# Kernel tuning notes

Hardware: AMD Instinct MI355X
Metric: run time of the kernel (lower is better)

Reference implementation:

```python
import jax, jax.numpy as jnp
import numpy as np

DIM = 192
BASE = 10000.0
DIM_X = DIM // 3
DIM_Y = DIM // 3
DIM_T = DIM - 2 * (DIM // 3)


def _inv_freq(d):
    return 1.0 / (BASE ** (jnp.arange(0, d, 2, dtype=jnp.float32) / d))


def setup_inputs() -> dict:
    key = jax.random.key(0)
    frames, height, width = 32, 64, 64
    x = jax.random.normal(key, (1, frames * height * width, DIM), dtype=jnp.float32)
    return {"x": x, "height": height, "width": width, "frames": frames}


def reference(x, height, width, frames):
    dtype = x.dtype
    # per-axis angle tables: [len, dim_axis/2] -> duplicated to [len, dim_axis]
    fx = jnp.arange(width, dtype=jnp.float32)[:, None] * _inv_freq(DIM_X)[None, :]
    fy = jnp.arange(height, dtype=jnp.float32)[:, None] * _inv_freq(DIM_Y)[None, :]
    ft = jnp.arange(frames, dtype=jnp.float32)[:, None] * _inv_freq(DIM_T)[None, :]
    fx = jnp.concatenate([fx, fx], axis=-1)  # [W, DIM_X]
    fy = jnp.concatenate([fy, fy], axis=-1)  # [H, DIM_Y]
    ft = jnp.concatenate([ft, ft], axis=-1)  # [T, DIM_T]

    def grid(ax, ay, at):
        # broadcast each axis table over the (T, H, W) grid, concat on feature dim
        gx = jnp.broadcast_to(ax[None, None, :, :], (frames, height, width, DIM_X))
        gy = jnp.broadcast_to(ay[None, :, None, :], (frames, height, width, DIM_Y))
        gt = jnp.broadcast_to(at[:, None, None, :], (frames, height, width, DIM_T))
        return jnp.concatenate([gx, gy, gt], axis=-1).reshape(frames * height * width, DIM)

    cos_3d = grid(jnp.cos(fx), jnp.cos(fy), jnp.cos(ft)).astype(dtype)
    sin_3d = grid(jnp.sin(fx), jnp.sin(fy), jnp.sin(ft)).astype(dtype)
    return (cos_3d, sin_3d)
```

## Files before the change

### kernel.cpp

```cpp
#include <hip/hip_runtime.h>


#define NPOS (32 * 64 * 64)
#define DIM 192

#define NEG_C (-0.41524101186092027f)
#define LOG2_INV_2PI (-2.6514961294723187f)
#define R1 0.7498942093324559f
#define R2 0.5623413251903491f
#define R3 0.4216965034285822f

__global__ __launch_bounds__(256) void rope3d_kernel(float* __restrict__ out) {
    const unsigned int i = blockIdx.x * 256u + threadIdx.x;
    const unsigned int r = i / 48u;
    const unsigned int c = i - r * 48u;

    const unsigned int t = r >> 12;
    const unsigned int h = (r >> 6) & 63u;
    const unsigned int w = r & 63u;

    const unsigned int axis = c >> 4;
    const float pos = (float)(axis == 0 ? w : (axis == 1 ? h : t));

    const unsigned int inner0 = (c * 4u) & 31u;
    const float fr0 = __builtin_exp2f(fmaf((float)inner0, NEG_C, LOG2_INV_2PI));
    const float fr1 = fr0 * R1;
    const float fr2 = fr0 * R2;
    const float fr3 = fr0 * R3;

    const float a0 = __builtin_amdgcn_fractf(pos * fr0);
    const float a1 = __builtin_amdgcn_fractf(pos * fr1);
    const float a2 = __builtin_amdgcn_fractf(pos * fr2);
    const float a3 = __builtin_amdgcn_fractf(pos * fr3);

    const float c0 = __builtin_amdgcn_cosf(a0);
    const float c1 = __builtin_amdgcn_cosf(a1);
    const float c2 = __builtin_amdgcn_cosf(a2);
    const float c3 = __builtin_amdgcn_cosf(a3);
    const float s0 = __builtin_amdgcn_sinf(a0);
    const float s1 = __builtin_amdgcn_sinf(a1);
    const float s2 = __builtin_amdgcn_sinf(a2);
    const float s3 = __builtin_amdgcn_sinf(a3);

    const size_t base = (size_t)i * 4u;
    *(float4*)(out + base) = make_float4(c0, c1, c2, c3);
    *(float4*)(out + (size_t)NPOS * DIM + base) = make_float4(s0, s1, s2, s3);
}

extern "C" void kernel_launch(void* const* d_in, const int* in_sizes, int n_in,
                              void* d_out, int out_size, void* d_ws, size_t ws_size,
                              hipStream_t stream) {
    (void)d_in; (void)in_sizes; (void)n_in; (void)d_ws; (void)ws_size; (void)out_size;
    float* out = (float*)d_out;
    const unsigned int total4 = NPOS * 48u;
    const unsigned int blocks = total4 / 256u;
    rope3d_kernel<<<blocks, 256, 0, stream>>>(out);
}
```

Before: 243.1 us.

## Use grid-stride loop reusing x/y sin-cos values across frame strides

Launches a fixed grid of 1536 blocks that loop over the output with a stride of two frames. The x and y axis angles are invariant under that stride, so their sin/cos are computed once and reused; only the time-axis columns recompute, with position advanced by two. This cuts transcendental work and block launch overhead, at the cost of a serial store loop per thread and less parallelism per store.

```diff
diff --git a/kernel.cpp b/kernel.cpp
--- a/kernel.cpp
+++ b/kernel.cpp
@@ -3,6 +3,11 @@
 
 #define NPOS (32 * 64 * 64)
 #define DIM 192
+#define TOTAL4 (NPOS * 48)
+#define NBLK 1536
+#define NTHR 256
+#define GSIZE (NBLK * NTHR)
+#define ITERS (TOTAL4 / GSIZE)
 
 #define NEG_C (-0.41524101186092027f)
 #define LOG2_INV_2PI (-2.6514961294723187f)
@@ -10,17 +15,11 @@
 #define R2 0.5623413251903491f
 #define R3 0.4216965034285822f
 
-__global__ __launch_bounds__(256) void rope3d_kernel(float* __restrict__ out) {
-    const unsigned int i = blockIdx.x * 256u + threadIdx.x;
-    const unsigned int r = i / 48u;
-    const unsigned int c = i - r * 48u;
-
-    const unsigned int t = r >> 12;
-    const unsigned int h = (r >> 6) & 63u;
-    const unsigned int w = r & 63u;
-
+__global__ __launch_bounds__(NTHR) void rope3d_kernel(float* __restrict__ out) {
+    const unsigned int g = blockIdx.x * NTHR + threadIdx.x;
+    const unsigned int r0 = g / 48u;
+    const unsigned int c = g - r0 * 48u;
     const unsigned int axis = c >> 4;
-    const float pos = (float)(axis == 0 ? w : (axis == 1 ? h : t));
 
     const unsigned int inner0 = (c * 4u) & 31u;
     const float fr0 = __builtin_exp2f(fmaf((float)inner0, NEG_C, LOG2_INV_2PI));
@@ -28,23 +27,41 @@
     const float fr2 = fr0 * R2;
     const float fr3 = fr0 * R3;
 
-    const float a0 = __builtin_amdgcn_fractf(pos * fr0);
-    const float a1 = __builtin_amdgcn_fractf(pos * fr1);
-    const float a2 = __builtin_amdgcn_fractf(pos * fr2);
-    const float a3 = __builtin_amdgcn_fractf(pos * fr3);
+    const unsigned int w = r0 & 63u;
+    const unsigned int h = (r0 >> 6) & 63u;
+    const unsigned int t = r0 >> 12;
+    float pos = (float)(axis == 0 ? w : (axis == 1 ? h : t));
 
-    const float c0 = __builtin_amdgcn_cosf(a0);
-    const float c1 = __builtin_amdgcn_cosf(a1);
-    const float c2 = __builtin_amdgcn_cosf(a2);
-    const float c3 = __builtin_amdgcn_cosf(a3);
-    const float s0 = __builtin_amdgcn_sinf(a0);
-    const float s1 = __builtin_amdgcn_sinf(a1);
-    const float s2 = __builtin_amdgcn_sinf(a2);
-    const float s3 = __builtin_amdgcn_sinf(a3);
+    float a0 = __builtin_amdgcn_fractf(pos * fr0);
+    float a1 = __builtin_amdgcn_fractf(pos * fr1);
+    float a2 = __builtin_amdgcn_fractf(pos * fr2);
+    float a3 = __builtin_amdgcn_fractf(pos * fr3);
+    float c0 = __builtin_amdgcn_cosf(a0), s0 = __builtin_amdgcn_sinf(a0);
+    float c1 = __builtin_amdgcn_cosf(a1), s1 = __builtin_amdgcn_sinf(a1);
+    float c2 = __builtin_amdgcn_cosf(a2), s2 = __builtin_amdgcn_sinf(a2);
+    float c3 = __builtin_amdgcn_cosf(a3), s3 = __builtin_amdgcn_sinf(a3);
 
-    const size_t base = (size_t)i * 4u;
-    *(float4*)(out + base) = make_float4(c0, c1, c2, c3);
-    *(float4*)(out + (size_t)NPOS * DIM + base) = make_float4(s0, s1, s2, s3);
+    float* pc = out + (size_t)g * 4u;
+    float* ps = out + (size_t)NPOS * DIM + (size_t)g * 4u;
+
+#pragma unroll 1
+    for (int k = 0; k < ITERS; ++k) {
+        *(float4*)pc = make_float4(c0, c1, c2, c3);
+        *(float4*)ps = make_float4(s0, s1, s2, s3);
+        pc += (size_t)GSIZE * 4u;
+        ps += (size_t)GSIZE * 4u;
+        if (axis == 2) {
+            pos += 2.0f;
+            a0 = __builtin_amdgcn_fractf(pos * fr0);
+            a1 = __builtin_amdgcn_fractf(pos * fr1);
+            a2 = __builtin_amdgcn_fractf(pos * fr2);
+            a3 = __builtin_amdgcn_fractf(pos * fr3);
+            c0 = __builtin_amdgcn_cosf(a0); s0 = __builtin_amdgcn_sinf(a0);
+            c1 = __builtin_amdgcn_cosf(a1); s1 = __builtin_amdgcn_sinf(a1);
+            c2 = __builtin_amdgcn_cosf(a2); s2 = __builtin_amdgcn_sinf(a2);
+            c3 = __builtin_amdgcn_cosf(a3); s3 = __builtin_amdgcn_sinf(a3);
+        }
+    }
 }
 
 extern "C" void kernel_launch(void* const* d_in, const int* in_sizes, int n_in,
@@ -52,7 +69,5 @@
                               hipStream_t stream) {
     (void)d_in; (void)in_sizes; (void)n_in; (void)d_ws; (void)ws_size; (void)out_size;
     float* out = (float*)d_out;
-    const unsigned int total4 = NPOS * 48u;
-    const unsigned int blocks = total4 / 256u;
-    rope3d_kernel<<<blocks, 256, 0, stream>>>(out);
+    rope3d_kernel<<<NBLK, NTHR, 0, stream>>>(out);
 }
```

Result: slower. 253.4 us (+4.3%).
